# Optimization experiments

Hardware: AMD Instinct MI355X
Metric: run time of the kernel (lower is better)

Reference implementation:

```python
import jax, jax.numpy as jnp
import numpy as np


def setup_inputs() -> dict:
    key = jax.random.key(0)
    ks = jax.random.split(key, 5)
    B, S, D, H, K = 2, 2048, 1024, 16, 64
    std = 0.02
    return {
        "x": jax.random.normal(ks[0], (B, S, D), dtype=jnp.float32),
        "W_Q": jax.random.normal(ks[1], (H, D, K), dtype=jnp.float32) * std,
        "W_K": jax.random.normal(ks[2], (H, D, K), dtype=jnp.float32) * std,
        "W_V": jax.random.normal(ks[3], (H, D, K), dtype=jnp.float32) * std,
        "W_O": jax.random.normal(ks[4], (H, K, D), dtype=jnp.float32) * std,
        "b_Q": jnp.zeros((H, K), dtype=jnp.float32),
        "b_K": jnp.zeros((H, K), dtype=jnp.float32),
        "b_V": jnp.zeros((H, K), dtype=jnp.float32),
        "b_O": jnp.zeros((D,), dtype=jnp.float32),
    }


def reference(x, W_Q, W_K, W_V, W_O, b_Q, b_K, b_V, b_O):
    # x: (B, S, D); W_*: (H, D, K); W_O: (H, K, D)
    S = x.shape[1]
    d_head = W_Q.shape[-1]
    q = jnp.einsum('bpd,hdk->bphk', x, W_Q) + b_Q
    k = jnp.einsum('bpd,hdk->bphk', x, W_K) + b_K
    v = jnp.einsum('bpd,hdk->bphk', x, W_V) + b_V
    scores = jnp.einsum('bphk,bqhk->bhpq', q, k) / jnp.sqrt(jnp.float32(d_head))
    # causal mask: positions q > p (strict upper triangle) are masked
    causal = jnp.tril(jnp.ones((S, S), dtype=bool))
    scores = jnp.where(causal, scores, jnp.float32(-jnp.inf))
    pattern = jax.nn.softmax(scores, axis=-1)
    z = jnp.einsum('bhpq,bqhk->bphk', pattern, v)
    out = jnp.einsum('bphk,hkd->bpd', z, W_O) + b_O
    return out
```

## Files before the change

kernel.cpp:

```cpp
#include <hip/hip_runtime.h>

typedef unsigned short u16;
typedef __attribute__((ext_vector_type(4))) float f32x4;
typedef __attribute__((ext_vector_type(8))) short s16x8;
typedef __attribute__((ext_vector_type(4))) unsigned short u16x4;
typedef __attribute__((ext_vector_type(2))) unsigned int u32x2;

#define S_ 2048
#define D_ 1024
#define H_ 16
#define KH 64
#define M_ 4096
#define BH_ 32

__device__ __forceinline__ float bf2f(u16 v) {
    union { unsigned int u; float f; } x; x.u = ((unsigned int)v) << 16; return x.f;
}
__device__ __forceinline__ u16 f2bf(float f) {
    union { float ff; unsigned int u; } x; x.ff = f;
    unsigned int r = x.u + 0x7fffu + ((x.u >> 16) & 1u);
    return (u16)(r >> 16);
}
__device__ __forceinline__ unsigned int cvt_pk_bf16(float lo, float hi) {
    unsigned int d;
    asm("v_cvt_pk_bf16_f32 %0, %1, %2" : "=v"(d) : "v"(lo), "v"(hi));
    return d;
}

__global__ void kcvt_x(const float* __restrict__ x, u16* __restrict__ xb) {
    const int i = (blockIdx.x * 256 + threadIdx.x) * 4;
    const float4 v = *(const float4*)&x[i];
    u16x4 o;
    o.x = f2bf(v.x); o.y = f2bf(v.y); o.z = f2bf(v.z); o.w = f2bf(v.w);
    *(u16x4*)&xb[i] = o;
}

__global__ void ktrans_w(const float* __restrict__ WQ, const float* __restrict__ WK,
                         const float* __restrict__ WV, const float* __restrict__ WO,
                         u16* __restrict__ wt) {
    __shared__ u16 tile[64][65];
    const int mat = blockIdx.z;
    const float* src = (mat == 0) ? WQ : (mat == 1) ? WK : (mat == 2) ? WV : WO;
    u16* dst = wt + (size_t)mat * 1048576;
    const int a0 = blockIdx.x * 64, b0 = blockIdx.y * 64;
    const int t = threadIdx.x;
    const int bl = t & 63, ar = t >> 6;
    #pragma unroll
    for (int i = 0; i < 16; ++i) {
        int a = a0 + i * 4 + ar, b = b0 + bl;
        size_t sa = (mat < 3) ? (((size_t)(b >> 6)) << 16) + ((size_t)a << 6) + (b & 63)
                              : (size_t)a * 1024 + b;
        tile[i * 4 + ar][bl] = f2bf(src[sa]);
    }
    __syncthreads();
    #pragma unroll
    for (int i = 0; i < 16; ++i) {
        int bl2 = i * 4 + ar;
        dst[(size_t)(b0 + bl2) * 1024 + a0 + bl] = tile[bl][bl2];
    }
}

__global__ __launch_bounds__(256)
void kgemm0(const u16* __restrict__ A, const u16* __restrict__ Wt,
            const float* __restrict__ b0p, const float* __restrict__ b1p,
            const float* __restrict__ b2p,
            u16* __restrict__ Qo, u16* __restrict__ Ko, u16* __restrict__ Vto) {
    __shared__ u16 As[2][128 * 32];
    __shared__ u16 Bs[2][128 * 32];
    const int t = threadIdx.x;
    const int l = t & 63, w = t >> 6;
    const int lq = l & 15, lg = l >> 4;
    const int wr = w >> 1, wc = w & 1;
    const int m0 = blockIdx.x * 128;
    const int n0 = blockIdx.y * 128;
    const int z = blockIdx.z;
    const u16* Bt = Wt + (size_t)z * 1048576;
    const float* bias = (z == 0) ? b0p : (z == 1) ? b1p : b2p;

    f32x4 acc[4][4] = {};

    auto stage = [&](int kt, int buf) {
        #pragma unroll
        for (int i = 0; i < 2; ++i) {
            int idx = t + i * 256;
            int row = idx >> 2, cc = idx & 3;
            const u16* ga = A + (size_t)(m0 + row) * 1024 + kt * 32 + cc * 8;
            const u16* gb = Bt + (size_t)(n0 + row) * 1024 + kt * 32 + cc * 8;
            __builtin_amdgcn_global_load_lds(
                (const __attribute__((address_space(1))) unsigned int*)ga,
                (__attribute__((address_space(3))) unsigned int*)(&As[buf][idx * 8]),
                16, 0, 0);
            __builtin_amdgcn_global_load_lds(
                (const __attribute__((address_space(1))) unsigned int*)gb,
                (__attribute__((address_space(3))) unsigned int*)(&Bs[buf][idx * 8]),
                16, 0, 0);
        }
    };

    stage(0, 0);
    __syncthreads();
    for (int kt = 0; kt < 32; ++kt) {
        const int cur = kt & 1;
        if (kt + 1 < 32) stage(kt + 1, cur ^ 1);
        s16x8 af[4], bf[4];
        #pragma unroll
        for (int m = 0; m < 4; ++m)
            af[m] = *(const s16x8*)&As[cur][(wr * 64 + m * 16 + lq) * 32 + lg * 8];
        #pragma unroll
        for (int n = 0; n < 4; ++n)
            bf[n] = *(const s16x8*)&Bs[cur][(wc * 64 + n * 16 + lq) * 32 + lg * 8];
        #pragma unroll
        for (int m = 0; m < 4; ++m)
            #pragma unroll
            for (int n = 0; n < 4; ++n)
                acc[m][n] = __builtin_amdgcn_mfma_f32_16x16x32_bf16(
                    bf[n], af[m], acc[m][n], 0, 0, 0);
        __syncthreads();
    }

    #pragma unroll
    for (int n = 0; n < 4; ++n) {
        const int gcolb = n0 + wc * 64 + n * 16 + lg * 4;
        const float4 bv = *(const float4*)&bias[gcolb];
        const int h = gcolb >> 6, kk0 = gcolb & 63;
        #pragma unroll
        for (int m = 0; m < 4; ++m) {
            const int grow = m0 + wr * 64 + m * 16 + lq;
            const int b = grow >> 11, s = grow & 2047;
            const float v0 = acc[m][n][0] + bv.x;
            const float v1 = acc[m][n][1] + bv.y;
            const float v2 = acc[m][n][2] + bv.z;
            const float v3 = acc[m][n][3] + bv.w;
            if (z == 2) {
                u16* vb = Vto + ((size_t)((b * 16 + h) * 64 + kk0) * 2048 + s);
                vb[0] = f2bf(v0); vb[2048] = f2bf(v1);
                vb[4096] = f2bf(v2); vb[6144] = f2bf(v3);
            } else {
                u16* outp = (z == 0) ? Qo : Ko;
                u32x2 wp;
                wp.x = cvt_pk_bf16(v0, v1);
                wp.y = cvt_pk_bf16(v2, v3);
                *(u32x2*)&outp[((size_t)(b * 16 + h) * 2048 + s) * 64 + kk0] = wp;
            }
        }
    }
}

__global__ __launch_bounds__(256)
void kgemm1(const u16* __restrict__ A, const u16* __restrict__ Bt,
            const float* __restrict__ bias, float* __restrict__ fo) {
    __shared__ u16 As[2][128 * 32];
    __shared__ u16 Bs[2][64 * 32];
    const int t = threadIdx.x;
    const int l = t & 63, w = t >> 6;
    const int lq = l & 15, lg = l >> 4;
    const int wr = w >> 1, wc = w & 1;

    const int lin = blockIdx.x;
    const int xcd = lin & 7;
    const int s = lin >> 3;
    const int nb = s & 15;
    const int mb = (s >> 4) * 8 + xcd;
    const int m0 = mb * 128;
    const int n0 = nb * 64;

    f32x4 acc[4][2] = {};

    auto stage = [&](int kt, int buf) {
        #pragma unroll
        for (int i = 0; i < 2; ++i) {
            int idx = t + i * 256;
            int row = idx >> 2, cc = idx & 3;
            __builtin_amdgcn_global_load_lds(
                (const __attribute__((address_space(1))) unsigned int*)
                    (A + (size_t)(m0 + row) * 1024 + kt * 32 + cc * 8),
                (__attribute__((address_space(3))) unsigned int*)(&As[buf][idx * 8]),
                16, 0, 0);
        }
        {
            int row = t >> 2, cc = t & 3;
            __builtin_amdgcn_global_load_lds(
                (const __attribute__((address_space(1))) unsigned int*)
                    (Bt + (size_t)(n0 + row) * 1024 + kt * 32 + cc * 8),
                (__attribute__((address_space(3))) unsigned int*)(&Bs[buf][t * 8]),
                16, 0, 0);
        }
    };

    stage(0, 0);
    __syncthreads();
    for (int kt = 0; kt < 32; ++kt) {
        const int cur = kt & 1;
        if (kt + 1 < 32) stage(kt + 1, cur ^ 1);
        s16x8 af[4], bf[2];
        #pragma unroll
        for (int m = 0; m < 4; ++m)
            af[m] = *(const s16x8*)&As[cur][(wr * 64 + m * 16 + lq) * 32 + lg * 8];
        #pragma unroll
        for (int n = 0; n < 2; ++n)
            bf[n] = *(const s16x8*)&Bs[cur][(wc * 32 + n * 16 + lq) * 32 + lg * 8];
        #pragma unroll
        for (int m = 0; m < 4; ++m)
            #pragma unroll
            for (int n = 0; n < 2; ++n)
                acc[m][n] = __builtin_amdgcn_mfma_f32_16x16x32_bf16(
                    bf[n], af[m], acc[m][n], 0, 0, 0);
        __syncthreads();
    }

    #pragma unroll
    for (int n = 0; n < 2; ++n) {
        const int gcolb = n0 + wc * 32 + n * 16 + lg * 4;
        const float4 bv = *(const float4*)&bias[gcolb];
        #pragma unroll
        for (int m = 0; m < 4; ++m) {
            const int grow = m0 + wr * 64 + m * 16 + lq;
            float4 o;
            o.x = acc[m][n][0] + bv.x;
            o.y = acc[m][n][1] + bv.y;
            o.z = acc[m][n][2] + bv.z;
            o.w = acc[m][n][3] + bv.w;
            *(float4*)&fo[(size_t)grow * 1024 + gcolb] = o;
        }
    }
}

__global__ __launch_bounds__(256)
void kattn(const u16* __restrict__ Q, const u16* __restrict__ K,
           const u16* __restrict__ Vt, u16* __restrict__ Z) {
    __shared__ u16 Ks[2][64 * 64];
    __shared__ u16 Vs[2][64 * 64];
    __shared__ u16 Pl[4][16 * 72];
    const int t = threadIdx.x, l = t & 63, w = t >> 6;
    const int lq = l & 15, lg = l >> 4;

    const int lin = blockIdx.x;
    const int xcd = lin & 7;
    const int r = lin >> 3;
    const int qt = 31 - (r >> 2);
    const int bh = xcd + 8 * (r & 3);

    const size_t base = (size_t)bh * (S_ * KH);
    const u16* Qb = Q + base;
    const u16* Kb = K + base;
    const u16* Vb = Vt + base;
    const int b = bh >> 4, h = bh & 15;
    u16* Pw = &Pl[w][0];

    const int c0 = ((lg ^ (lq & 7)) * 8);
    const int c1 = c0 ^ 32;
    const float NINF = -__builtin_inff();
    const float SCL = 0.18033688011112042f;

    auto stage = [&](int k0, int buf) {
        #pragma unroll
        for (int i = 0; i < 2; ++i) {
            const int idx2 = t + i * 256;
            const int row = idx2 >> 3;
            const int cg = (idx2 & 7) ^ (row & 7);
            __builtin_amdgcn_global_load_lds(
                (const __attribute__((address_space(1))) unsigned int*)
                    (Kb + (size_t)(k0 + row) * KH + cg * 8),
                (__attribute__((address_space(3))) unsigned int*)(&Ks[buf][idx2 * 8]),
                16, 0, 0);
            __builtin_amdgcn_global_load_lds(
                (const __attribute__((address_space(1))) unsigned int*)
                    (Vb + (size_t)row * S_ + k0 + cg * 8),
                (__attribute__((address_space(3))) unsigned int*)(&Vs[buf][idx2 * 8]),
                16, 0, 0);
        }
    };

    const int nt = qt + 1;
    const int qs = qt * 64 + w * 16;
    const int lim = w * 16 + lq;

    const s16x8 qf0 = *(const s16x8*)&Qb[(size_t)(qs + lq) * KH + lg * 8];
    const s16x8 qf1 = *(const s16x8*)&Qb[(size_t)(qs + lq) * KH + 32 + lg * 8];

    float mrow = NINF, lrow = 0.f;
    f32x4 zacc[4] = {};

    stage(0, 0);
    __syncthreads();

    for (int kt = 0; kt < nt; ++kt) {
        const int buf = kt & 1;
        if (kt + 1 < nt) stage((kt + 1) * 64, buf ^ 1);

        f32x4 sf[4] = {};
        __builtin_amdgcn_s_setprio(1);
        #pragma unroll
        for (int kf = 0; kf < 4; ++kf) {
            const int row = kf * 16 + lq;
            const s16x8 ka = *(const s16x8*)&Ks[buf][row * 64 + c0];
            const s16x8 kb = *(const s16x8*)&Ks[buf][row * 64 + c1];
            sf[kf] = __builtin_amdgcn_mfma_f32_16x16x32_bf16(ka, qf0, sf[kf], 0, 0, 0);
            sf[kf] = __builtin_amdgcn_mfma_f32_16x16x32_bf16(kb, qf1, sf[kf], 0, 0, 0);
        }
        __builtin_amdgcn_s_setprio(0);

        float p[4][4];
        const bool diag = (kt == qt);
        #pragma unroll
        for (int kf = 0; kf < 4; ++kf)
            #pragma unroll
            for (int r2 = 0; r2 < 4; ++r2) {
                float v = sf[kf][r2] * SCL;
                if (diag && (kf * 16 + lg * 4 + r2) > lim) v = NINF;
                p[kf][r2] = v;
            }

        float mk[4];
        #pragma unroll
        for (int kf = 0; kf < 4; ++kf)
            mk[kf] = fmaxf(fmaxf(p[kf][0], p[kf][1]), fmaxf(p[kf][2], p[kf][3]));
        float tmax = fmaxf(fmaxf(mk[0], mk[1]), fmaxf(mk[2], mk[3]));
        tmax = fmaxf(tmax, __shfl_xor(tmax, 16));
        tmax = fmaxf(tmax, __shfl_xor(tmax, 32));

        float alpha = 1.f;
        if (!__all(tmax <= mrow + 8.f)) {
            const float nm = fmaxf(mrow, tmax);
            alpha = exp2f(mrow - nm);
            mrow = nm;
            #pragma unroll
            for (int nf = 0; nf < 4; ++nf)
                #pragma unroll
                for (int r2 = 0; r2 < 4; ++r2)
                    zacc[nf][r2] *= alpha;
        }

        float sk[4];
        #pragma unroll
        for (int kf = 0; kf < 4; ++kf) {
            #pragma unroll
            for (int r2 = 0; r2 < 4; ++r2)
                p[kf][r2] = exp2f(p[kf][r2] - mrow);
            sk[kf] = (p[kf][0] + p[kf][1]) + (p[kf][2] + p[kf][3]);
        }
        float rsum = (sk[0] + sk[1]) + (sk[2] + sk[3]);
        rsum += __shfl_xor(rsum, 16);
        rsum += __shfl_xor(rsum, 32);
        lrow = lrow * alpha + rsum;

        #pragma unroll
        for (int kf = 0; kf < 4; ++kf) {
            u32x2 wp;
            wp.x = cvt_pk_bf16(p[kf][0], p[kf][1]);
            wp.y = cvt_pk_bf16(p[kf][2], p[kf][3]);
            *(u32x2*)&Pw[lq * 72 + kf * 16 + lg * 4] = wp;
        }
        const s16x8 pa0 = *(const s16x8*)&Pw[lq * 72 + lg * 8];
        const s16x8 pa1 = *(const s16x8*)&Pw[lq * 72 + 32 + lg * 8];

        __builtin_amdgcn_s_setprio(1);
        #pragma unroll
        for (int nf = 0; nf < 4; ++nf) {
            const int row = nf * 16 + lq;
            const s16x8 v0 = *(const s16x8*)&Vs[buf][row * 64 + c0];
            const s16x8 v1 = *(const s16x8*)&Vs[buf][row * 64 + c1];
            zacc[nf] = __builtin_amdgcn_mfma_f32_16x16x32_bf16(v0, pa0, zacc[nf], 0, 0, 0);
            zacc[nf] = __builtin_amdgcn_mfma_f32_16x16x32_bf16(v1, pa1, zacc[nf], 0, 0, 0);
        }
        __builtin_amdgcn_s_setprio(0);
        __syncthreads();
    }

    const float rinv = 1.f / lrow;
    const size_t zrow = (size_t)(b * S_ + qs + lq) * 1024 + h * 64;
    #pragma unroll
    for (int nf = 0; nf < 4; ++nf) {
        u32x2 wp;
        wp.x = cvt_pk_bf16(zacc[nf][0] * rinv, zacc[nf][1] * rinv);
        wp.y = cvt_pk_bf16(zacc[nf][2] * rinv, zacc[nf][3] * rinv);
        *(u32x2*)&Z[zrow + nf * 16 + lg * 4] = wp;
    }
}

extern "C" void kernel_launch(void* const* d_in, const int* in_sizes, int n_in,
                              void* d_out, int out_size, void* d_ws, size_t ws_size,
                              hipStream_t stream) {
    const float* x  = (const float*)d_in[0];
    const float* WQ = (const float*)d_in[1];
    const float* WK = (const float*)d_in[2];
    const float* WV = (const float*)d_in[3];
    const float* WO = (const float*)d_in[4];
    const float* bQ = (const float*)d_in[5];
    const float* bK = (const float*)d_in[6];
    const float* bV = (const float*)d_in[7];
    const float* bO = (const float*)d_in[8];
    float* out = (float*)d_out;

    u16* ws  = (u16*)d_ws;
    u16* xb  = ws;
    u16* wt  = xb + 4194304u;
    u16* Qb  = wt + 4194304u;
    u16* Kb  = Qb + 4194304u;
    u16* Vtb = Kb + 4194304u;
    u16* Zb  = Vtb + 4194304u;

    kcvt_x<<<dim3(4096), 256, 0, stream>>>(x, xb);
    ktrans_w<<<dim3(16, 16, 4), 256, 0, stream>>>(WQ, WK, WV, WO, wt);
    kgemm0<<<dim3(32, 8, 3), 256, 0, stream>>>(
        xb, wt, bQ, bK, bV, Qb, Kb, Vtb);
    kattn<<<dim3(1024), 256, 0, stream>>>(Qb, Kb, Vtb, Zb);
    kgemm1<<<dim3(512), 256, 0, stream>>>(
        Zb, wt + 3u * 1048576u, bO, out);
}
```

Before: 199.8 us.

## Fold softmax scale into Q projection, compute row sums via MFMA, retile output GEMM

The Q projection epilogue now applies the softmax scale (including the log2e factor) so the attention loop no longer multiplies every score. In the attention kernel a constant row of ones is appended to the V tile, so an extra MFMA accumulates the softmax denominator and the per-tile sum and shuffle reductions go away. Because P is rounded to bf16 before that MFMA, the denominator is now summed from rounded values rather than fp32 ones. The output projection GEMM moves to 128x128 tiles with K=64 steps and XOR-swizzled LDS, halving the grid and remapping blocks to XCDs, which adds LDS use and may lower occupancy.

New measurement: 200.1 us. About the same (+0.2%).

```diff
diff --git a/kernel.cpp b/kernel.cpp
--- a/kernel.cpp
+++ b/kernel.cpp
@@ -76,6 +76,7 @@
     const int z = blockIdx.z;
     const u16* Bt = Wt + (size_t)z * 1048576;
     const float* bias = (z == 0) ? b0p : (z == 1) ? b1p : b2p;
+    const float oscl = (z == 0) ? 0.18033688011112042f : 1.f;
 
     f32x4 acc[4][4] = {};
 
@@ -127,10 +128,10 @@
         for (int m = 0; m < 4; ++m) {
             const int grow = m0 + wr * 64 + m * 16 + lq;
             const int b = grow >> 11, s = grow & 2047;
-            const float v0 = acc[m][n][0] + bv.x;
-            const float v1 = acc[m][n][1] + bv.y;
-            const float v2 = acc[m][n][2] + bv.z;
-            const float v3 = acc[m][n][3] + bv.w;
+            const float v0 = (acc[m][n][0] + bv.x) * oscl;
+            const float v1 = (acc[m][n][1] + bv.y) * oscl;
+            const float v2 = (acc[m][n][2] + bv.z) * oscl;
+            const float v3 = (acc[m][n][3] + bv.w) * oscl;
             if (z == 2) {
                 u16* vb = Vto + ((size_t)((b * 16 + h) * 64 + kk0) * 2048 + s);
                 vb[0] = f2bf(v0); vb[2048] = f2bf(v1);
@@ -149,8 +150,8 @@
 __global__ __launch_bounds__(256)
 void kgemm1(const u16* __restrict__ A, const u16* __restrict__ Bt,
             const float* __restrict__ bias, float* __restrict__ fo) {
-    __shared__ u16 As[2][128 * 32];
-    __shared__ u16 Bs[2][64 * 32];
+    __shared__ u16 As[2][128 * 64];
+    __shared__ u16 Bs[2][128 * 64];
     const int t = threadIdx.x;
     const int l = t & 63, w = t >> 6;
     const int lq = l & 15, lg = l >> 4;
@@ -158,59 +159,65 @@
 
     const int lin = blockIdx.x;
     const int xcd = lin & 7;
-    const int s = lin >> 3;
-    const int nb = s & 15;
-    const int mb = (s >> 4) * 8 + xcd;
-    const int m0 = mb * 128;
-    const int n0 = nb * 64;
-
-    f32x4 acc[4][2] = {};
+    const int r = lin >> 3;
+    const int mb = 4 * xcd + (r & 3);
+    const int nb = r >> 2;
+    const int m0 = mb * 128, n0 = nb * 128;
+
+    f32x4 acc[4][4] = {};
 
     auto stage = [&](int kt, int buf) {
         #pragma unroll
-        for (int i = 0; i < 2; ++i) {
-            int idx = t + i * 256;
-            int row = idx >> 2, cc = idx & 3;
+        for (int i = 0; i < 4; ++i) {
+            const int idx = t + i * 256;
+            const int row = idx >> 3;
+            const int cg = (idx & 7) ^ (row & 7);
             __builtin_amdgcn_global_load_lds(
                 (const __attribute__((address_space(1))) unsigned int*)
-                    (A + (size_t)(m0 + row) * 1024 + kt * 32 + cc * 8),
+                    (A + (size_t)(m0 + row) * 1024 + kt * 64 + cg * 8),
                 (__attribute__((address_space(3))) unsigned int*)(&As[buf][idx * 8]),
                 16, 0, 0);
-        }
-        {
-            int row = t >> 2, cc = t & 3;
             __builtin_amdgcn_global_load_lds(
                 (const __attribute__((address_space(1))) unsigned int*)
-                    (Bt + (size_t)(n0 + row) * 1024 + kt * 32 + cc * 8),
-                (__attribute__((address_space(3))) unsigned int*)(&Bs[buf][t * 8]),
+                    (Bt + (size_t)(n0 + row) * 1024 + kt * 64 + cg * 8),
+                (__attribute__((address_space(3))) unsigned int*)(&Bs[buf][idx * 8]),
                 16, 0, 0);
         }
     };
 
     stage(0, 0);
     __syncthreads();
-    for (int kt = 0; kt < 32; ++kt) {
+    for (int kt = 0; kt < 16; ++kt) {
         const int cur = kt & 1;
-        if (kt + 1 < 32) stage(kt + 1, cur ^ 1);
-        s16x8 af[4], bf[2];
-        #pragma unroll
-        for (int m = 0; m < 4; ++m)
-            af[m] = *(const s16x8*)&As[cur][(wr * 64 + m * 16 + lq) * 32 + lg * 8];
-        #pragma unroll
-        for (int n = 0; n < 2; ++n)
-            bf[n] = *(const s16x8*)&Bs[cur][(wc * 32 + n * 16 + lq) * 32 + lg * 8];
-        #pragma unroll
-        for (int m = 0; m < 4; ++m)
-            #pragma unroll
-            for (int n = 0; n < 2; ++n)
-                acc[m][n] = __builtin_amdgcn_mfma_f32_16x16x32_bf16(
-                    bf[n], af[m], acc[m][n], 0, 0, 0);
+        if (kt + 1 < 16) stage(kt + 1, cur ^ 1);
+        #pragma unroll
+        for (int kk = 0; kk < 2; ++kk) {
+            s16x8 af[4], bf[4];
+            #pragma unroll
+            for (int m = 0; m < 4; ++m) {
+                const int row = wr * 64 + m * 16 + lq;
+                const int c = ((kk * 4 + lg) ^ (lq & 7)) * 8;
+                af[m] = *(const s16x8*)&As[cur][row * 64 + c];
+            }
+            #pragma unroll
+            for (int n = 0; n < 4; ++n) {
+                const int row = wc * 64 + n * 16 + lq;
+                const int c = ((kk * 4 + lg) ^ (lq & 7)) * 8;
+                bf[n] = *(const s16x8*)&Bs[cur][row * 64 + c];
+            }
+            #pragma unroll
+            for (int m = 0; m < 4; ++m)
+                #pragma unroll
+                for (int n = 0; n < 4; ++n)
+                    acc[m][n] = __builtin_amdgcn_mfma_f32_16x16x32_bf16(
+                        bf[n], af[m], acc[m][n], 0, 0, 0);
+        }
         __syncthreads();
     }
 
     #pragma unroll
-    for (int n = 0; n < 2; ++n) {
-        const int gcolb = n0 + wc * 32 + n * 16 + lg * 4;
+    for (int n = 0; n < 4; ++n) {
+        const int gcolb = n0 + wc * 64 + n * 16 + lg * 4;
         const float4 bv = *(const float4*)&bias[gcolb];
         #pragma unroll
         for (int m = 0; m < 4; ++m) {
@@ -229,7 +236,7 @@
 void kattn(const u16* __restrict__ Q, const u16* __restrict__ K,
            const u16* __restrict__ Vt, u16* __restrict__ Z) {
     __shared__ u16 Ks[2][64 * 64];
-    __shared__ u16 Vs[2][64 * 64];
+    __shared__ u16 Vs[2][80 * 64];
     __shared__ u16 Pl[4][16 * 72];
     const int t = threadIdx.x, l = t & 63, w = t >> 6;
     const int lq = l & 15, lg = l >> 4;
@@ -250,7 +257,12 @@
     const int c0 = ((lg ^ (lq & 7)) * 8);
     const int c1 = c0 ^ 32;
     const float NINF = -__builtin_inff();
-    const float SCL = 0.18033688011112042f;
+
+    for (int i = t; i < 2048; i += 256) {
+        const int bufi = i >> 10, rem = i & 1023;
+        const int row = 64 + (rem >> 6), col = rem & 63;
+        Vs[bufi][row * 64 + col] = (row == 64) ? (u16)0x3F80 : (u16)0;
+    }
 
     auto stage = [&](int k0, int buf) {
         #pragma unroll
@@ -278,8 +290,8 @@
     const s16x8 qf0 = *(const s16x8*)&Qb[(size_t)(qs + lq) * KH + lg * 8];
     const s16x8 qf1 = *(const s16x8*)&Qb[(size_t)(qs + lq) * KH + 32 + lg * 8];
 
-    float mrow = NINF, lrow = 0.f;
-    f32x4 zacc[4] = {};
+    float mrow = NINF;
+    f32x4 zacc[5] = {};
 
     stage(0, 0);
     __syncthreads();
@@ -300,55 +312,44 @@
         }
         __builtin_amdgcn_s_setprio(0);
 
-        float p[4][4];
-        const bool diag = (kt == qt);
+        if (kt == qt) {
+            #pragma unroll
+            for (int kf = 0; kf < 4; ++kf)
+                #pragma unroll
+                for (int r2 = 0; r2 < 4; ++r2)
+                    if ((kf * 16 + lg * 4 + r2) > lim) sf[kf][r2] = NINF;
+        }
+
+        float mk[4];
         #pragma unroll
         for (int kf = 0; kf < 4; ++kf)
-            #pragma unroll
-            for (int r2 = 0; r2 < 4; ++r2) {
-                float v = sf[kf][r2] * SCL;
-                if (diag && (kf * 16 + lg * 4 + r2) > lim) v = NINF;
-                p[kf][r2] = v;
-            }
-
-        float mk[4];
-        #pragma unroll
-        for (int kf = 0; kf < 4; ++kf)
-            mk[kf] = fmaxf(fmaxf(p[kf][0], p[kf][1]), fmaxf(p[kf][2], p[kf][3]));
+            mk[kf] = fmaxf(fmaxf(sf[kf][0], sf[kf][1]), fmaxf(sf[kf][2], sf[kf][3]));
         float tmax = fmaxf(fmaxf(mk[0], mk[1]), fmaxf(mk[2], mk[3]));
         tmax = fmaxf(tmax, __shfl_xor(tmax, 16));
         tmax = fmaxf(tmax, __shfl_xor(tmax, 32));
 
-        float alpha = 1.f;
         if (!__all(tmax <= mrow + 8.f)) {
             const float nm = fmaxf(mrow, tmax);
-            alpha = exp2f(mrow - nm);
+            const float alpha = exp2f(mrow - nm);
             mrow = nm;
             #pragma unroll
-            for (int nf = 0; nf < 4; ++nf)
+            for (int nf = 0; nf < 5; ++nf)
                 #pragma unroll
                 for (int r2 = 0; r2 < 4; ++r2)
                     zacc[nf][r2] *= alpha;
         }
 
-        float sk[4];
-        #pragma unroll
-        for (int kf = 0; kf < 4; ++kf) {
+        #pragma unroll
+        for (int kf = 0; kf < 4; ++kf)
             #pragma unroll
             for (int r2 = 0; r2 < 4; ++r2)
-                p[kf][r2] = exp2f(p[kf][r2] - mrow);
-            sk[kf] = (p[kf][0] + p[kf][1]) + (p[kf][2] + p[kf][3]);
-        }
-        float rsum = (sk[0] + sk[1]) + (sk[2] + sk[3]);
-        rsum += __shfl_xor(rsum, 16);
-        rsum += __shfl_xor(rsum, 32);
-        lrow = lrow * alpha + rsum;
+                sf[kf][r2] = exp2f(sf[kf][r2] - mrow);
 
         #pragma unroll
         for (int kf = 0; kf < 4; ++kf) {
             u32x2 wp;
-            wp.x = cvt_pk_bf16(p[kf][0], p[kf][1]);
-            wp.y = cvt_pk_bf16(p[kf][2], p[kf][3]);
+            wp.x = cvt_pk_bf16(sf[kf][0], sf[kf][1]);
+            wp.y = cvt_pk_bf16(sf[kf][2], sf[kf][3]);
             *(u32x2*)&Pw[lq * 72 + kf * 16 + lg * 4] = wp;
         }
         const s16x8 pa0 = *(const s16x8*)&Pw[lq * 72 + lg * 8];
@@ -356,7 +357,7 @@
 
         __builtin_amdgcn_s_setprio(1);
         #pragma unroll
-        for (int nf = 0; nf < 4; ++nf) {
+        for (int nf = 0; nf < 5; ++nf) {
             const int row = nf * 16 + lq;
             const s16x8 v0 = *(const s16x8*)&Vs[buf][row * 64 + c0];
             const s16x8 v1 = *(const s16x8*)&Vs[buf][row * 64 + c1];
@@ -367,7 +368,8 @@
         __syncthreads();
     }
 
-    const float rinv = 1.f / lrow;
+    const float denom = __shfl(zacc[4][0], lq);
+    const float rinv = 1.f / denom;
     const size_t zrow = (size_t)(b * S_ + qs + lq) * 1024 + h * 64;
     #pragma unroll
     for (int nf = 0; nf < 4; ++nf) {
@@ -405,6 +407,6 @@
     kgemm0<<<dim3(32, 8, 3), 256, 0, stream>>>(
         xb, wt, bQ, bK, bV, Qb, Kb, Vtb);
     kattn<<<dim3(1024), 256, 0, stream>>>(Qb, Kb, Vtb, Zb);
-    kgemm1<<<dim3(512), 256, 0, stream>>>(
+    kgemm1<<<dim3(256), 256, 0, stream>>>(
         Zb, wt + 3u * 1048576u, bO, out);
 }
```
